# Kernel tuning notes

Hardware: AMD Instinct MI355X
Metric: run time of the kernel (lower is better)

The kernel has to match this reference:

```python
import jax, jax.numpy as jnp
import numpy as np

N = 50000   # nodes
E = 800000  # edges (avg degree 16)
C = 64      # in_channels == out_channels


def _linear_params(key, fan_in, fan_out):
    kw, kb = jax.random.split(key)
    s = 1.0 / np.sqrt(fan_in)
    W = jax.random.uniform(kw, (fan_out, fan_in), minval=-s, maxval=s, dtype=jnp.float32)
    b = jax.random.uniform(kb, (fan_out,), minval=-s, maxval=s, dtype=jnp.float32)
    return W, b


def setup_inputs() -> dict:
    key = jax.random.key(0)
    ks = jax.random.split(key, 12)
    scalar = jax.random.normal(ks[0], (N, C), dtype=jnp.float32)
    vector = jax.random.normal(ks[1], (N, 3, C), dtype=jnp.float32)
    position = jax.random.normal(ks[2], (N, 3), dtype=jnp.float32)
    edge_index = jax.random.randint(ks[3], (2, E), 0, N, dtype=jnp.int64)
    edge_attr = jax.random.uniform(ks[4], (E,), dtype=jnp.float32)
    # Scalar_Conv params
    Wss, bss = _linear_params(ks[5], 2 * C, C)   # s_to_s
    Wvs, bvs = _linear_params(ks[6], 2 * C, C)   # v_to_s
    Wsl, bsl = _linear_params(ks[7], 2 * C, C)   # scalar_linear
    # Vector_Conv params
    Wsv, bsv = _linear_params(ks[8], 2 * C, C)   # s_to_v
    Wvv, bvv = _linear_params(ks[9], 2 * C, C)   # v_to_v
    Wvl, bvl = _linear_params(ks[10], 2 * C, C)  # vector_linear
    return dict(scalar=scalar, vector=vector, position=position,
                edge_index=edge_index, edge_attr=edge_attr,
                Wss=Wss, bss=bss, Wvs=Wvs, bvs=bvs, Wsl=Wsl, bsl=bsl,
                Wsv=Wsv, bsv=bsv, Wvv=Wvv, bvv=bvv, Wvl=Wvl, bvl=bvl)


def _norm(edge_index, edge_attr, num_nodes):
    # B=True path: edge_attr-weighted symmetric degree normalization
    row, col = edge_index[0], edge_index[1]
    deg = jax.ops.segment_sum(edge_attr, col, num_segments=num_nodes)
    deg_safe = jnp.where(deg > 0, deg, 1.0)
    dis = jnp.where(deg > 0, deg_safe ** -0.5, 0.0)
    return row, col, dis[row] * dis[col] * edge_attr


def _forward(scalar, vector, position, edge_index, edge_attr,
             Wss, bss, Wvs, bvs, Wsl, bsl, Wsv, bsv, Wvv, bvv, Wvl, bvl):
    num_nodes = scalar.shape[0]
    row, col = _norm(edge_index, edge_attr, num_nodes)[:2]
    _, _, norm = _norm(edge_index, edge_attr, num_nodes)
    # PyG: _i = target (col), _j = source (row); aggregate at col
    s_i, s_j = scalar[col], scalar[row]            # [E,C]
    v_i, v_j = vector[col], vector[row]            # [E,3,C]
    pos = position[col] - position[row]            # [E,3]
    s_cat = jnp.concatenate([s_i, s_j], axis=-1)   # [E,2C]
    v_cat = jnp.concatenate([v_i, v_j], axis=-1)   # [E,3,2C]

    # ---- Scalar_Conv messages ----
    s2s = jax.nn.silu(s_cat @ Wss.T + bss)                          # [E,C]
    v2s = v_cat @ Wvs.T + bvs                                       # [E,3,C]
    v2s = jax.nn.silu(jnp.sum(v2s * pos[:, :, None], axis=1))       # [E,C]
    s_msg = (jnp.concatenate([s2s, v2s], axis=-1) @ Wsl.T + bsl)    # [E,C]
    s_msg = norm[:, None] * s_msg
    s_agg = jax.ops.segment_sum(s_msg, col, num_segments=num_nodes)

    # ---- Vector_Conv messages ----
    s2v = s_cat @ Wsv.T + bsv                                       # [E,C]
    s2v = jnp.tanh(s2v[:, None, :] * pos[:, :, None])               # [E,3,C]
    v2v = v_cat @ Wvv.T + bvv                                       # [E,3,C]
    v_msg = jnp.concatenate([v2v, s2v], axis=-1) @ Wvl.T + bvl      # [E,3,C]
    v_msg = norm[:, None, None] * v_msg
    v_agg = jax.ops.segment_sum(v_msg, col, num_segments=num_nodes)

    scalar_out = jax.nn.silu(s_agg) + scalar
    vector_out = jnp.tanh(v_agg) + vector
    return scalar_out, vector_out


def reference(scalar, vector, position, edge_index, edge_attr,
              Wss, bss, Wvs, bvs, Wsl, bsl, Wsv, bsv, Wvv, bvv, Wvl, bvl):
    return _forward(scalar, vector, position, edge_index, edge_attr,
                    Wss, bss, Wvs, bvs, Wsl, bsl, Wsv, bsv, Wvv, bvv, Wvl, bvl)
```

## Files before the change

### kernel.cpp

```cpp
#include <hip/hip_runtime.h>
#include <cstdint>
#include <cstddef>

typedef unsigned int   u32;
typedef unsigned short u16;
typedef __attribute__((ext_vector_type(8))) short bf16x8;
typedef __attribute__((ext_vector_type(4))) float f32x4;

__device__ __forceinline__ float bf2f(u32 bits16) { return __uint_as_float(bits16 << 16); }
__device__ __forceinline__ u16 f2bf(float f) {
  u32 u = __float_as_uint(f);
  u = u + 0x7FFFu + ((u >> 16) & 1u);
  return (u16)(u >> 16);
}
__device__ __forceinline__ u32 pk(float a, float b) {
  return (u32)f2bf(a) | ((u32)f2bf(b) << 16);
}
__device__ __forceinline__ float lo16(u32 w) { return bf2f(w & 0xFFFFu); }
__device__ __forceinline__ float hi16(u32 w) { return bf2f(w >> 16); }
__device__ __forceinline__ float frcp(float x) { return __builtin_amdgcn_rcpf(x); }
__device__ __forceinline__ float fexp2(float x) { return __builtin_amdgcn_exp2f(x); }

#define NL2E   (-1.4426950408889634f)
#define TWOL2E (2.8853900817779268f)
#define CNTSC  1073741824.0

__device__ __forceinline__ int load_idx(const int* eidx, int is64, long long pos) {
  if (is64) return (int)(((const long long*)eidx)[pos]);
  return eidx[pos];
}

__global__ void k_prep1(const float* Wvl, const float* Wvv,
                        const float* bvv, const float* bvl,
                        const int* eidx, int E, int* flag,
                        float* WcTmp, float* bc,
                        double* dpk, int* erecI, int* tilestat, int* tilectr,
                        int N, int NB) {
  int b = blockIdx.x, tid = threadIdx.x;
  if (b < 32) {
    int c = 2 * b + (tid >> 7), kk = tid & 127;
    float s = 0.f;
    for (int m = 0; m < 64; ++m) s += Wvl[c * 128 + m] * Wvv[m * 128 + kk];
    WcTmp[c * 128 + kk] = s;
  } else if (b == 32) {
    __shared__ int zc;
    if (tid == 0) zc = 0;
    __syncthreads();
    int n = (E < 1024) ? E : 1024;
    int local = 0;
    for (int i = tid; i < n; i += 256) {
      if (eidx[2 * i + 1] == 0) local++;
    }
    atomicAdd(&zc, local);
    __syncthreads();
    if (tid == 0) *flag = (zc >= (n >> 1)) ? 1 : 0;
  } else if (b == 33) {
    if (tid < 64) {
      float s = 0.f;
      for (int m = 0; m < 64; ++m) s += Wvl[tid * 128 + m] * bvv[m];
      bc[tid] = s + bvl[tid];
    }
  } else if (b == 34) {
    if (tid < 64) erecI[E + tid] = 0;
    if (tid == 64) *tilectr = 0;
    for (int i = tid; i < NB; i += 256) tilestat[i] = 0;
  } else {
    int idx = (b - 35) * 256 + tid;
    if (idx < N) dpk[idx] = 0.0;
  }
}

__global__ void k_prep2(const float* Wss, const float* Wsv, const float* Wvs,
                        const float* Wsl, const float* Wvl, const float* WcTmp,
                        u32* Wsl2, u32* Wpk, u16* Wtg) {
  int b = blockIdx.x, tid = threadIdx.x;
  if (b < 2) {
    for (int i = 0; i < 8; ++i) {
      int o = b * 2048 + i * 256 + tid;
      int h = o & 1, c = (o >> 1) & 63, g = o >> 7;
      int k = 4 * g + 2 * h;
      Wsl2[o] = pk(Wsl[c * 128 + k], Wsl[c * 128 + k + 1]);
    }
  } else if (b == 2) {
    for (int i = 0; i < 8; ++i) {
      int o = i * 256 + tid;
      int h = o & 1, c = (o >> 1) & 63, g = o >> 7;
      int k = 4 * g + 2 * h;
      Wpk[o] = pk(Wvl[c * 128 + 64 + k], Wvl[c * 128 + 64 + k + 1]);
    }
  } else {
    for (int i = 0; i < 16; ++i) {
      int p = (b - 3) * 4096 + i * 256 + tid;
      int r = p >> 6, k = p & 63;
      int g = (r >> 6) & 3, ch = r & 63;
      int src = ch * 128 + ((g & 2) ? 64 : 0) + k;
      float w;
      if (r < 256) w = (g & 1) ? Wsv[src] : Wss[src];
      else         w = (g & 1) ? WcTmp[src] : Wvs[src];
      u16 h = f2bf(w);
      Wtg[r * 128 + k] = h;
      Wtg[r * 128 + 64 + k] = f2bf(w - bf2f(h));
    }
  }
}

__global__ void k_scan(const double* dpk, float* dis, int* rowptr, int* cursor,
                       int* tilestat, int* tilectr, int N, int E) {
  __shared__ int lds[256];
  __shared__ int sTile, sPrefix;
  int tid = threadIdx.x;
  if (tid == 0) sTile = atomicAdd(tilectr, 1);
  __syncthreads();
  int tile = sTile;
  int idx = tile * 256 + tid;
  int c = 0;
  if (idx < N) {
    double p = dpk[idx];
    c = (int)(p * (1.0 / CNTSC));
    float dg = (float)(p - (double)c * CNTSC);
    dis[idx] = (dg > 0.f) ? rsqrtf(dg) : 0.f;
  }
  lds[tid] = c;
  __syncthreads();
  for (int off = 1; off < 256; off <<= 1) {
    int t = (tid >= off) ? lds[tid - off] : 0;
    __syncthreads();
    lds[tid] += t;
    __syncthreads();
  }
  int incl = lds[tid];
  int aggregate = lds[255];
  if (tile == 0) {
    if (tid == 0) {
      atomicExch(&tilestat[0], (2 << 30) | aggregate);
      rowptr[N] = E;
      sPrefix = 0;
    }
  } else {
    if (tid == 0) atomicExch(&tilestat[tile], (1 << 30) | aggregate);
    if (tid < 64) {
      int pred = tile - 1 - tid;
      int excl;
      while (true) {
        int s = (pred >= 0) ? atomicAdd(&tilestat[pred], 0) : (2 << 30);
        u32 fl = (u32)s >> 30;
        unsigned long long pfx = __ballot(fl == 2);
        unsigned long long unp = __ballot(fl == 0);
        int l1 = pfx ? (__ffsll((long long)pfx) - 1) : 64;
        int l0 = unp ? (__ffsll((long long)unp) - 1) : 64;
        if (l1 < 64 && l0 > l1) {
          int v = (tid <= l1) ? (s & 0x3FFFFFFF) : 0;
          #pragma unroll
          for (int o = 32; o > 0; o >>= 1) v += __shfl_xor(v, o, 64);
          excl = v;
          break;
        }
      }
      if (tid == 0) {
        sPrefix = excl;
        atomicExch(&tilestat[tile], (2 << 30) | (excl + aggregate));
      }
    }
  }
  __syncthreads();
  int exclPrefix = sPrefix;
  if (idx < N) {
    int o = exclPrefix + incl - c;
    rowptr[idx] = o;
    cursor[idx] = o;
  }
}

__device__ __forceinline__ void gemm_body(
    u32* smem, int tid, int nb,
    const float* __restrict__ scalar, const float* __restrict__ vector,
    const u16* __restrict__ Wtg,
    uint4* __restrict__ rec_i4, uint4* __restrict__ rec_j4, int N) {
  u16*   Ax = (u16*)smem;
  float* Ep = (float*)smem;
  int lane = tid & 63, wv = tid >> 6;

  {
    int srow = tid >> 2, skq = tid & 3;
    const float* sp;
    int snode;
    if (srow < 32) { snode = nb + srow; sp = scalar + (size_t)snode * 64 + skq * 16; }
    else {
      int d = (srow - 32) >> 5, nl2 = (srow - 32) & 31;
      snode = nb + nl2;
      sp = vector + (size_t)snode * 192 + d * 64 + skq * 16;
    }
    bool valid = snode < N;
    u16 hi[16], lo[16];
    #pragma unroll
    for (int q = 0; q < 4; ++q) {
      float4 v = valid ? *(const float4*)(sp + 4 * q) : make_float4(0.f, 0.f, 0.f, 0.f);
      float xs[4] = {v.x, v.y, v.z, v.w};
      #pragma unroll
      for (int j = 0; j < 4; ++j) {
        u16 h = f2bf(xs[j]);
        hi[4 * q + j] = h;
        lo[4 * q + j] = f2bf(xs[j] - bf2f(h));
      }
    }
    int rs = srow & 7;
    #pragma unroll
    for (int c = 0; c < 2; ++c) {
      int lc = 2 * skq + c;
      uint4 wh, wl;
      wh.x = (u32)hi[8*c+0] | ((u32)hi[8*c+1] << 16);
      wh.y = (u32)hi[8*c+2] | ((u32)hi[8*c+3] << 16);
      wh.z = (u32)hi[8*c+4] | ((u32)hi[8*c+5] << 16);
      wh.w = (u32)hi[8*c+6] | ((u32)hi[8*c+7] << 16);
      wl.x = (u32)lo[8*c+0] | ((u32)lo[8*c+1] << 16);
      wl.y = (u32)lo[8*c+2] | ((u32)lo[8*c+3] << 16);
      wl.z = (u32)lo[8*c+4] | ((u32)lo[8*c+5] << 16);
      wl.w = (u32)lo[8*c+6] | ((u32)lo[8*c+7] << 16);
      *(uint4*)(Ax + srow * 128 + (lc ^ rs) * 8)        = wh;
      *(uint4*)(Ax + srow * 128 + ((8 + lc) ^ rs) * 8)  = wl;
    }
  }
  __syncthreads();

  int c0 = wv * 32;
  int bl = lane & 15, bh = lane >> 4;
  f32x4 acc[8][2];
  #pragma unroll
  for (int mt = 0; mt < 8; ++mt)
    #pragma unroll
    for (int nt = 0; nt < 2; ++nt)
      acc[mt][nt] = (f32x4){0.f, 0.f, 0.f, 0.f};

  #pragma unroll
  for (int kh = 0; kh < 2; ++kh) {
    int k0 = kh * 32;
    bf16x8 Bh[2][2], Bl[2][2];
    #pragma unroll
    for (int rg = 0; rg < 2; ++rg)
      #pragma unroll
      for (int nt = 0; nt < 2; ++nt) {
        size_t rr = (size_t)(rg * 256 + c0 + nt * 16 + bl) * 128 + k0 + bh * 8;
        Bh[rg][nt] = *(const bf16x8*)(Wtg + rr);
        Bl[rg][nt] = *(const bf16x8*)(Wtg + rr + 64);
      }
    #pragma unroll
    for (int mt = 0; mt < 8; ++mt) {
      int row = mt * 16 + bl;
      int ch = (k0 >> 3) + bh, rs = row & 7;
      bf16x8 Ah = *(const bf16x8*)(Ax + row * 128 + (ch ^ rs) * 8);
      bf16x8 Al = *(const bf16x8*)(Ax + row * 128 + ((8 + ch) ^ rs) * 8);
      int rg = (mt < 2) ? 0 : 1;
      #pragma unroll
      for (int nt = 0; nt < 2; ++nt) {
        f32x4 a = acc[mt][nt];
        a = __builtin_amdgcn_mfma_f32_16x16x32_bf16(Ah, Bh[rg][nt], a, 0, 0, 0);
        a = __builtin_amdgcn_mfma_f32_16x16x32_bf16(Al, Bh[rg][nt], a, 0, 0, 0);
        a = __builtin_amdgcn_mfma_f32_16x16x32_bf16(Ah, Bl[rg][nt], a, 0, 0, 0);
        acc[mt][nt] = a;
      }
    }
  }

  int ech = tid & 63, eng = tid >> 6;
  uint4 oi[4], oj[4];
  #pragma unroll
  for (int pg = 0; pg < 4; ++pg) {
    __syncthreads();
    #pragma unroll
    for (int mm = 0; mm < 2; ++mm) {
      int mt = 2 * pg + mm;
      #pragma unroll
      for (int nt = 0; nt < 2; ++nt)
        #pragma unroll
        for (int r = 0; r < 4; ++r) {
          int rl = mm * 16 + bh * 4 + r;
          Ep[rl * 256 + c0 + nt * 16 + bl] = acc[mt][nt][r];
        }
    }
    __syncthreads();
    #pragma unroll
    for (int q = 0; q < 4; ++q) {
      int nl2 = eng + 8 * q;
      float vi0 = Ep[nl2 * 256 + ech];
      float vi1 = Ep[nl2 * 256 + 64 + ech];
      float vj0 = Ep[nl2 * 256 + 128 + ech];
      float vj1 = Ep[nl2 * 256 + 192 + ech];
      if (pg == 0) {
        oi[q].x = pk(vi0, vi1);                  oj[q].x = pk(vj0, vj1);
      } else if (pg == 1) {
        oi[q].y = (u32)f2bf(vi0);                oj[q].y = (u32)f2bf(vj0);
        oi[q].z = (u32)f2bf(vi1) << 16;          oj[q].z = (u32)f2bf(vj1) << 16;
      } else if (pg == 2) {
        oi[q].y |= (u32)f2bf(vi0) << 16;         oj[q].y |= (u32)f2bf(vj0) << 16;
        oi[q].w = (u32)f2bf(vi1);                oj[q].w = (u32)f2bf(vj1);
      } else {
        oi[q].z |= (u32)f2bf(vi0);               oj[q].z |= (u32)f2bf(vj0);
        oi[q].w |= (u32)f2bf(vi1) << 16;         oj[q].w |= (u32)f2bf(vj1) << 16;
      }
    }
  }
  #pragma unroll
  for (int q = 0; q < 4; ++q) {
    int node = nb + eng + 8 * q;
    if (node < N) {
      rec_i4[(size_t)node * 64 + ech] = oi[q];
      rec_j4[(size_t)node * 64 + ech] = oj[q];
    }
  }
}

__global__ __launch_bounds__(512, 4) void k_gemm_deg(
    const float* __restrict__ scalar, const float* __restrict__ vector,
    const u16* __restrict__ Wtg,
    uint4* __restrict__ rec_i4, uint4* __restrict__ rec_j4, int N, int GB1,
    const int* __restrict__ eidx, const int* __restrict__ flag,
    const float* __restrict__ attr, double* __restrict__ dpk, int E) {
  __shared__ u32 smem[8192];
  int tid = threadIdx.x;
  if ((int)blockIdx.x >= GB1) {
    int e = ((int)blockIdx.x - GB1) * 512 + tid;
    if (e < E) {
      int is64 = *flag;
      int col = load_idx(eidx, is64, (long long)E + e);
      atomicAdd(&dpk[col], (double)attr[e] + CNTSC);
    }
    return;
  }
  gemm_body(smem, tid, (int)blockIdx.x * 32, scalar, vector, Wtg, rec_i4, rec_j4, N);
}

__global__ __launch_bounds__(512, 4) void k_gemm_fill(
    const float* __restrict__ scalar, const float* __restrict__ vector,
    const u16* __restrict__ Wtg,
    uint4* __restrict__ rec_i4, uint4* __restrict__ rec_j4, int N, int GB1, int GB2,
    const int* __restrict__ eidx, const int* __restrict__ flag,
    const float* __restrict__ attr, const float* __restrict__ dis,
    const float* __restrict__ pos, int* __restrict__ cursor,
    float4* __restrict__ erecA, int* __restrict__ erecI, int E) {
  __shared__ u32 smem[8192];
  int tid = threadIdx.x;
  if ((int)blockIdx.x >= GB2) {
    int e = ((int)blockIdx.x - GB2) * 512 + tid;
    if (e < E) {
      int is64 = *flag;
      int r  = load_idx(eidx, is64, e);
      int cl = load_idx(eidx, is64, (long long)E + e);
      float wr = dis[r] * attr[e];
      float dx = pos[cl * 3 + 0] - pos[r * 3 + 0];
      float dy = pos[cl * 3 + 1] - pos[r * 3 + 1];
      float dz = pos[cl * 3 + 2] - pos[r * 3 + 2];
      int p = atomicAdd(&cursor[cl], 1);
      erecA[p] = make_float4(wr, dx, dy, dz);
      erecI[p] = r;
    }
    return;
  }
  gemm_body(smem, tid, (GB1 + (int)blockIdx.x) * 32, scalar, vector, Wtg, rec_i4, rec_j4, N);
}

__global__ __launch_bounds__(512) void k_edges(
    const u16* __restrict__ rec_i, const u16* __restrict__ rec_j,
    const float4* __restrict__ erecA, const int* __restrict__ erecI,
    const int* __restrict__ rowptr, const float* __restrict__ dis,
    const float* __restrict__ scalar, const float* __restrict__ vector,
    const float* __restrict__ bss, const float* __restrict__ bvs,
    const float* __restrict__ bsv, const float* __restrict__ bsl,
    const u32* __restrict__ Wsl2g, const u32* __restrict__ Wpkg,
    const float* __restrict__ bcg,
    float* __restrict__ out_s, float* __restrict__ out_v, int N) {
  __shared__ u32 sWsl[4096];
  __shared__ u32 sWv[2048];
  __shared__ float sStage[8 * 192];
  int tid = threadIdx.x, lane = tid & 63, wv = tid >> 6;
  for (int o = tid; o < 4096; o += 512) sWsl[o] = Wsl2g[o];
  for (int o = tid; o < 2048; o += 512) sWv[o] = Wpkg[o];
  __syncthreads();

  int node = __builtin_amdgcn_readfirstlane((int)(blockIdx.x * 8) + wv);
  if (node >= N) node = N - 1;

  uint4 riv = *(const uint4*)(rec_i + ((size_t)node << 9) + lane * 8);
  float aiB  = lo16(riv.x) + bss[lane];
  float KciB = TWOL2E * (hi16(riv.x) + bsv[lane]);
  float Bvs  = bvs[lane];
  float bib0 = lo16(riv.y) + Bvs;
  float bib1 = hi16(riv.y) + Bvs;
  float bib2 = lo16(riv.z) + Bvs;
  float Pi0  = hi16(riv.z), Pi1 = lo16(riv.w), Pi2 = hi16(riv.w);
  float bsl_c = bsl[lane], bc_c = bcg[lane];
  float disc = dis[node];

  float us = 0, uv = 0, t0 = 0, t1 = 0, t2 = 0, g0 = 0, g1 = 0, g2 = 0, wa = 0;
  int rp = rowptr[node], re = rowptr[node + 1];
  u32 lane16 = (u32)lane << 4;
  const char* rjb = (const char*)rec_j;

  u32 ra = (u32)erecI[rp];
  u32 rb = (u32)erecI[rp + 1];
  uint4 pre0 = *(const uint4*)(rjb + ((ra << 10) + lane16));
  uint4 pre1 = *(const uint4*)(rjb + ((rb << 10) + lane16));
  int p = rp;
  #define EDGE_MATH(CUR, EV)                                                  \
    {                                                                         \
      float nrm = EV.x, dx = EV.y, dy = EV.z, dz = EV.w;                      \
      float aj  = lo16(CUR.x), cj  = hi16(CUR.x);                             \
      float bj0 = lo16(CUR.y), bj1 = hi16(CUR.y), bj2 = lo16(CUR.z);          \
      float rj0 = hi16(CUR.z), rj1 = lo16(CUR.w), rj2 = hi16(CUR.w);          \
      float xs  = aiB + aj;                                                   \
      float s2s = xs * frcp(1.f + fexp2(xs * NL2E));                          \
      float yv  = (bib0 + bj0) * dx;                                          \
      yv = fmaf(bib1 + bj1, dy, yv);                                          \
      yv = fmaf(bib2 + bj2, dz, yv);                                          \
      float v2s = yv * frcp(1.f + fexp2(yv * NL2E));                          \
      float qh  = fmaf(TWOL2E, cj, KciB);                                     \
      float th0 = fmaf(-2.f, frcp(1.f + fexp2(qh * dx)), 1.f);                \
      float th1 = fmaf(-2.f, frcp(1.f + fexp2(qh * dy)), 1.f);                \
      float th2 = fmaf(-2.f, frcp(1.f + fexp2(qh * dz)), 1.f);                \
      us = fmaf(nrm, s2s, us); uv = fmaf(nrm, v2s, uv);                       \
      t0 = fmaf(nrm, th0, t0); t1 = fmaf(nrm, th1, t1); t2 = fmaf(nrm, th2, t2);\
      g0 = fmaf(nrm, rj0, g0); g1 = fmaf(nrm, rj1, g1); g2 = fmaf(nrm, rj2, g2);\
      wa += nrm;                                                              \
    }
  for (; p + 1 < re; p += 2) {
    uint4 cur0 = pre0, cur1 = pre1;
    u32 rn0 = (u32)erecI[p + 2];
    u32 rn1 = (u32)erecI[p + 3];
    pre0 = *(const uint4*)(rjb + ((rn0 << 10) + lane16));
    pre1 = *(const uint4*)(rjb + ((rn1 << 10) + lane16));
    float4 e0 = erecA[p];
    float4 e1 = erecA[p + 1];
    EDGE_MATH(cur0, e0)
    EDGE_MATH(cur1, e1)
  }
  if (p < re) {
    uint4 cur0 = pre0;
    float4 e0 = erecA[p];
    EDGE_MATH(cur0, e0)
  }
  #undef EDGE_MATH

  us *= disc; uv *= disc;
  t0 *= disc; t1 *= disc; t2 *= disc;
  g0 *= disc; g1 *= disc; g2 *= disc;
  wa *= disc;

  float* mys = &sStage[wv * 192];
  mys[lane] = us; mys[64 + lane] = uv;
  __threadfence_block();
  float acc = wa * bsl_c;
  #pragma unroll
  for (int g = 0; g < 32; ++g) {
    float4 u = *(const float4*)&mys[4 * g];
    uint2 w = *(const uint2*)&sWsl[(g * 64 + lane) * 2];
    acc = fmaf(u.x, lo16(w.x), acc);
    acc = fmaf(u.y, hi16(w.x), acc);
    acc = fmaf(u.z, lo16(w.y), acc);
    acc = fmaf(u.w, hi16(w.y), acc);
  }
  size_t so = ((size_t)node << 6) + lane;
  out_s[so] = acc * frcp(1.f + fexp2(acc * NL2E)) + scalar[so];

  __threadfence_block();
  mys[lane] = t0; mys[64 + lane] = t1; mys[128 + lane] = t2;
  __threadfence_block();
  float a20 = fmaf(wa, bc_c + Pi0, g0);
  float a21 = fmaf(wa, bc_c + Pi1, g1);
  float a22 = fmaf(wa, bc_c + Pi2, g2);
  #pragma unroll
  for (int g = 0; g < 16; ++g) {
    float4 u0 = *(const float4*)&mys[4 * g];
    float4 u1 = *(const float4*)&mys[64 + 4 * g];
    float4 u2 = *(const float4*)&mys[128 + 4 * g];
    uint2 w = *(const uint2*)&sWv[(g * 64 + lane) * 2];
    float w0 = lo16(w.x), w1 = hi16(w.x), w2 = lo16(w.y), w3 = hi16(w.y);
    a20 = fmaf(u0.x, w0, a20); a20 = fmaf(u0.y, w1, a20);
    a20 = fmaf(u0.z, w2, a20); a20 = fmaf(u0.w, w3, a20);
    a21 = fmaf(u1.x, w0, a21); a21 = fmaf(u1.y, w1, a21);
    a21 = fmaf(u1.z, w2, a21); a21 = fmaf(u1.w, w3, a21);
    a22 = fmaf(u2.x, w0, a22); a22 = fmaf(u2.y, w1, a22);
    a22 = fmaf(u2.z, w2, a22); a22 = fmaf(u2.w, w3, a22);
  }
  float a2v[3] = {a20, a21, a22};
  #pragma unroll
  for (int d = 0; d < 3; ++d) {
    size_t vo = (((size_t)node * 3 + d) << 6) + lane;
    float th = fmaf(-2.f, frcp(1.f + fexp2(TWOL2E * a2v[d])), 1.f);
    out_v[vo] = th + vector[vo];
  }
}

extern "C" void kernel_launch(void* const* d_in, const int* in_sizes, int n_in,
                              void* d_out, int out_size, void* d_ws, size_t ws_size,
                              hipStream_t stream) {
  const float* scalar   = (const float*)d_in[0];
  const float* vector   = (const float*)d_in[1];
  const float* position = (const float*)d_in[2];
  const int*   eidx     = (const int*)d_in[3];
  const float* attr     = (const float*)d_in[4];
  const float* Wss = (const float*)d_in[5];
  const float* bss = (const float*)d_in[6];
  const float* Wvs = (const float*)d_in[7];
  const float* bvs = (const float*)d_in[8];
  const float* Wsl = (const float*)d_in[9];
  const float* bsl = (const float*)d_in[10];
  const float* Wsv = (const float*)d_in[11];
  const float* bsv = (const float*)d_in[12];
  const float* Wvv = (const float*)d_in[13];
  const float* bvv = (const float*)d_in[14];
  const float* Wvl = (const float*)d_in[15];
  const float* bvl = (const float*)d_in[16];

  int N = in_sizes[0] / 64;
  int E = in_sizes[4];
  int NB = (N + 255) / 256;

  char* wsb = (char*)d_ws;
  size_t off = 0;
  auto alloc = [&](size_t bytes) -> char* {
    char* p = wsb + off;
    off += (bytes + 255) & ~(size_t)255;
    return p;
  };
  double* dpk    = (double*)alloc((size_t)N * 8);
  int*    rowptr = (int*)alloc((size_t)(N + 1) * 4);
  int*    cursor = (int*)alloc((size_t)N * 4);
  float*  dis    = (float*)alloc((size_t)N * 4);
  int*    tilestat = (int*)alloc((size_t)NB * 4);
  int*    tilectr  = (int*)alloc(4);
  float4* erecA  = (float4*)alloc((size_t)E * 16);
  int*    erecI  = (int*)alloc((size_t)(E + 64) * 4);
  u16*    rec_i  = (u16*)alloc((size_t)N * 512 * 2);
  u16*    rec_j  = (u16*)alloc((size_t)N * 512 * 2);
  u16*    Wtg    = (u16*)alloc(512 * 128 * 2);
  u32*    Wsl2   = (u32*)alloc(4096 * 4);
  u32*    Wpk    = (u32*)alloc(2048 * 4);
  float*  WcTmp  = (float*)alloc(64 * 128 * 4);
  float*  bc     = (float*)alloc(64 * 4);
  int*    flag   = (int*)alloc(4);
  (void)ws_size; (void)n_in; (void)out_size;

  int GB  = (N + 31) / 32;
  int GB1 = GB / 2;
  int GB2 = GB - GB1;
  int DB  = (E + 511) / 512;

  k_prep1<<<35 + NB, 256, 0, stream>>>(Wvl, Wvv, bvv, bvl, eidx, E, flag,
                                       WcTmp, bc, dpk, erecI, tilestat, tilectr, N, NB);
  k_prep2<<<11, 256, 0, stream>>>(Wss, Wsv, Wvs, Wsl, Wvl, WcTmp, Wsl2, Wpk, Wtg);
  k_gemm_deg<<<GB1 + DB, 512, 0, stream>>>(scalar, vector, Wtg,
                                           (uint4*)rec_i, (uint4*)rec_j, N, GB1,
                                           eidx, flag, attr, dpk, E);
  k_scan<<<NB, 256, 0, stream>>>(dpk, dis, rowptr, cursor, tilestat, tilectr, N, E);
  k_gemm_fill<<<GB2 + DB, 512, 0, stream>>>(scalar, vector, Wtg,
                                            (uint4*)rec_i, (uint4*)rec_j, N, GB1, GB2,
                                            eidx, flag, attr, dis, position, cursor,
                                            erecA, erecI, E);
  k_edges<<<(N + 7) / 8, 512, 0, stream>>>(rec_i, rec_j, erecA, erecI, rowptr, dis,
                                           scalar, vector, bss, bvs, bsv, bsl,
                                           Wsl2, Wpk, bc,
                                           (float*)d_out, (float*)d_out + (size_t)N * 64, N);
}
```

Baseline: 407.0 us.

## Merge prep kernels and pack degree accumulation into integer 64-bit atomics

Fuses the two weight-preparation kernels into one launch: blocks that need the combined Wvl·Wvv matrix now compute it into shared memory instead of going through a global temporary. The degree/count accumulator switches from double-precision atomics to a packed u64 integer (count in the high bits, fixed-point weighted degree in the low 42 bits). This saves a kernel launch and replaces FP64 atomic adds with integer ones. In exchange, the degree is quantised to about 2^-26 resolution and each block recomputes its part of the 64x64x64 product redundantly.

```diff
diff --git a/kernel.cpp b/kernel.cpp
--- a/kernel.cpp
+++ b/kernel.cpp
@@ -4,6 +4,7 @@
 
 typedef unsigned int   u32;
 typedef unsigned short u16;
+typedef unsigned long long u64;
 typedef __attribute__((ext_vector_type(8))) short bf16x8;
 typedef __attribute__((ext_vector_type(4))) float f32x4;
 
@@ -23,26 +24,31 @@
 
 #define NL2E   (-1.4426950408889634f)
 #define TWOL2E (2.8853900817779268f)
-#define CNTSC  1073741824.0
+#define DEGSC    67108864.0f
+#define DEGSCINV 1.4901161193847656e-8f
+#define DEGMASK  0x3FFFFFFFFFFull
 
 __device__ __forceinline__ int load_idx(const int* eidx, int is64, long long pos) {
   if (is64) return (int)(((const long long*)eidx)[pos]);
   return eidx[pos];
 }
 
-__global__ void k_prep1(const float* Wvl, const float* Wvv,
-                        const float* bvv, const float* bvl,
-                        const int* eidx, int E, int* flag,
-                        float* WcTmp, float* bc,
-                        double* dpk, int* erecI, int* tilestat, int* tilectr,
-                        int N, int NB) {
+__global__ void k_prep(const float* Wss, const float* Wsv, const float* Wvs,
+                       const float* Wsl, const float* Wvl, const float* Wvv,
+                       const float* bvv, const float* bvl,
+                       const int* eidx, int E, int* flag, float* bc,
+                       u32* Wsl2, u32* Wpk, u16* Wtg,
+                       u64* dpk, int* erecI, int* tilestat, int* tilectr,
+                       int N, int NB) {
+  __shared__ float Wcs[4096];
   int b = blockIdx.x, tid = threadIdx.x;
-  if (b < 32) {
-    int c = 2 * b + (tid >> 7), kk = tid & 127;
-    float s = 0.f;
-    for (int m = 0; m < 64; ++m) s += Wvl[c * 128 + m] * Wvv[m * 128 + kk];
-    WcTmp[c * 128 + kk] = s;
-  } else if (b == 32) {
+  if (b == 0) {
+    if (tid < 64) {
+      float s = 0.f;
+      for (int m = 0; m < 64; ++m) s += Wvl[tid * 128 + m] * bvv[m];
+      bc[tid] = s + bvl[tid];
+    }
+  } else if (b == 1) {
     __shared__ int zc;
     if (tid == 0) zc = 0;
     __syncthreads();
@@ -54,57 +60,58 @@
     atomicAdd(&zc, local);
     __syncthreads();
     if (tid == 0) *flag = (zc >= (n >> 1)) ? 1 : 0;
-  } else if (b == 33) {
-    if (tid < 64) {
-      float s = 0.f;
-      for (int m = 0; m < 64; ++m) s += Wvl[tid * 128 + m] * bvv[m];
-      bc[tid] = s + bvl[tid];
-    }
-  } else if (b == 34) {
+  } else if (b == 2) {
     if (tid < 64) erecI[E + tid] = 0;
     if (tid == 64) *tilectr = 0;
     for (int i = tid; i < NB; i += 256) tilestat[i] = 0;
-  } else {
-    int idx = (b - 35) * 256 + tid;
-    if (idx < N) dpk[idx] = 0.0;
-  }
-}
-
-__global__ void k_prep2(const float* Wss, const float* Wsv, const float* Wvs,
-                        const float* Wsl, const float* Wvl, const float* WcTmp,
-                        u32* Wsl2, u32* Wpk, u16* Wtg) {
-  int b = blockIdx.x, tid = threadIdx.x;
-  if (b < 2) {
+  } else if (b < 5) {
     for (int i = 0; i < 8; ++i) {
-      int o = b * 2048 + i * 256 + tid;
+      int o = (b - 3) * 2048 + i * 256 + tid;
       int h = o & 1, c = (o >> 1) & 63, g = o >> 7;
       int k = 4 * g + 2 * h;
       Wsl2[o] = pk(Wsl[c * 128 + k], Wsl[c * 128 + k + 1]);
     }
-  } else if (b == 2) {
+  } else if (b == 5) {
     for (int i = 0; i < 8; ++i) {
       int o = i * 256 + tid;
       int h = o & 1, c = (o >> 1) & 63, g = o >> 7;
       int k = 4 * g + 2 * h;
       Wpk[o] = pk(Wvl[c * 128 + 64 + k], Wvl[c * 128 + 64 + k + 1]);
     }
-  } else {
+  } else if (b < 14) {
+    int w = b - 6;
+    bool needWc = (w == 5) || (w == 7);
+    if (needWc) {
+      int off = (w == 7) ? 64 : 0;
+      for (int i = 0; i < 16; ++i) {
+        int q = i * 256 + tid;
+        int ch = q >> 6, k = q & 63;
+        float s = 0.f;
+        for (int m = 0; m < 64; ++m) s += Wvl[ch * 128 + m] * Wvv[m * 128 + off + k];
+        Wcs[ch * 64 + k] = s;
+      }
+      __syncthreads();
+    }
     for (int i = 0; i < 16; ++i) {
-      int p = (b - 3) * 4096 + i * 256 + tid;
+      int p = w * 4096 + i * 256 + tid;
       int r = p >> 6, k = p & 63;
       int g = (r >> 6) & 3, ch = r & 63;
       int src = ch * 128 + ((g & 2) ? 64 : 0) + k;
-      float w;
-      if (r < 256) w = (g & 1) ? Wsv[src] : Wss[src];
-      else         w = (g & 1) ? WcTmp[src] : Wvs[src];
-      u16 h = f2bf(w);
+      float wv;
+      if (needWc)       wv = Wcs[ch * 64 + k];
+      else if (r < 256) wv = (g & 1) ? Wsv[src] : Wss[src];
+      else              wv = Wvs[src];
+      u16 h = f2bf(wv);
       Wtg[r * 128 + k] = h;
-      Wtg[r * 128 + 64 + k] = f2bf(w - bf2f(h));
-    }
-  }
-}
-
-__global__ void k_scan(const double* dpk, float* dis, int* rowptr, int* cursor,
+      Wtg[r * 128 + 64 + k] = f2bf(wv - bf2f(h));
+    }
+  } else {
+    int idx = (b - 14) * 256 + tid;
+    if (idx < N) dpk[idx] = 0ull;
+  }
+}
+
+__global__ void k_scan(const u64* dpk, float* dis, int* rowptr, int* cursor,
                        int* tilestat, int* tilectr, int N, int E) {
   __shared__ int lds[256];
   __shared__ int sTile, sPrefix;
@@ -115,9 +122,9 @@
   int idx = tile * 256 + tid;
   int c = 0;
   if (idx < N) {
-    double p = dpk[idx];
-    c = (int)(p * (1.0 / CNTSC));
-    float dg = (float)(p - (double)c * CNTSC);
+    u64 p = dpk[idx];
+    c = (int)(p >> 42);
+    float dg = (float)(p & DEGMASK) * DEGSCINV;
     dis[idx] = (dg > 0.f) ? rsqrtf(dg) : 0.f;
   }
   lds[tid] = c;
@@ -314,7 +321,7 @@
     const u16* __restrict__ Wtg,
     uint4* __restrict__ rec_i4, uint4* __restrict__ rec_j4, int N, int GB1,
     const int* __restrict__ eidx, const int* __restrict__ flag,
-    const float* __restrict__ attr, double* __restrict__ dpk, int E) {
+    const float* __restrict__ attr, u64* __restrict__ dpk, int E) {
   __shared__ u32 smem[8192];
   int tid = threadIdx.x;
   if ((int)blockIdx.x >= GB1) {
@@ -322,7 +329,8 @@
     if (e < E) {
       int is64 = *flag;
       int col = load_idx(eidx, is64, (long long)E + e);
-      atomicAdd(&dpk[col], (double)attr[e] + CNTSC);
+      u64 val = (1ull << 42) | (u64)(attr[e] * DEGSC);
+      atomicAdd(&dpk[col], val);
     }
     return;
   }
@@ -521,7 +529,7 @@
     off += (bytes + 255) & ~(size_t)255;
     return p;
   };
-  double* dpk    = (double*)alloc((size_t)N * 8);
+  u64*    dpk    = (u64*)alloc((size_t)N * 8);
   int*    rowptr = (int*)alloc((size_t)(N + 1) * 4);
   int*    cursor = (int*)alloc((size_t)N * 4);
   float*  dis    = (float*)alloc((size_t)N * 4);
@@ -534,7 +542,6 @@
   u16*    Wtg    = (u16*)alloc(512 * 128 * 2);
   u32*    Wsl2   = (u32*)alloc(4096 * 4);
   u32*    Wpk    = (u32*)alloc(2048 * 4);
-  float*  WcTmp  = (float*)alloc(64 * 128 * 4);
   float*  bc     = (float*)alloc(64 * 4);
   int*    flag   = (int*)alloc(4);
   (void)ws_size; (void)n_in; (void)out_size;
@@ -544,9 +551,9 @@
   int GB2 = GB - GB1;
   int DB  = (E + 511) / 512;
 
-  k_prep1<<<35 + NB, 256, 0, stream>>>(Wvl, Wvv, bvv, bvl, eidx, E, flag,
-                                       WcTmp, bc, dpk, erecI, tilestat, tilectr, N, NB);
-  k_prep2<<<11, 256, 0, stream>>>(Wss, Wsv, Wvs, Wsl, Wvl, WcTmp, Wsl2, Wpk, Wtg);
+  k_prep<<<14 + NB, 256, 0, stream>>>(Wss, Wsv, Wvs, Wsl, Wvl, Wvv, bvv, bvl,
+                                      eidx, E, flag, bc, Wsl2, Wpk, Wtg,
+                                      dpk, erecI, tilestat, tilectr, N, NB);
   k_gemm_deg<<<GB1 + DB, 512, 0, stream>>>(scalar, vector, Wtg,
                                            (uint4*)rec_i, (uint4*)rec_j, N, GB1,
                                            eidx, flag, attr, dpk, E);
```

New measurement: 427.8 us. +5.1%, slower.
